# Optimization experiments

Hardware: AMD Instinct MI355X
Metric: run time of the kernel (lower is better)

Reference implementation:

```python
import jax, jax.numpy as jnp
import numpy as np

L1, L2, B, D = 512, 512, 32, 768
EPS = 1e-8

def setup_inputs() -> dict:
    key = jax.random.key(0)
    k1, k2 = jax.random.split(key)
    return {
        "x1": jax.random.normal(k1, (L1, B, D), dtype=jnp.float32),
        "x1_mask": jnp.ones((L1, B), dtype=jnp.float32),
        "x2": jax.random.normal(k2, (L2, B, D), dtype=jnp.float32),
        "x2_mask": jnp.ones((L2, B), dtype=jnp.float32),
    }

def reference(x1, x1_mask, x2, x2_mask):
    # to batch-major: [B, L, D]
    x1b = jnp.transpose(x1, (1, 0, 2))
    x2b = jnp.transpose(x2, (1, 0, 2))
    m1 = jnp.transpose(x1_mask, (1, 0))  # [B, L1]
    m2 = jnp.transpose(x2_mask, (1, 0))  # [B, L2]

    # raw scores [B, L1, L2]
    scores = jnp.einsum('bld,bmd->blm', x1b, x2b)

    # x1 attends over x2: softmax over axis 2 with x2 mask
    w2 = jnp.exp(scores - jnp.max(scores, axis=2, keepdims=True))
    w2 = w2 * m2[:, None, :]
    alpha = w2 / (jnp.sum(w2, axis=-1, keepdims=True) + EPS)  # [B, L1, L2]
    x1_dual = jnp.einsum('blm,bmd->bld', alpha, x2b)           # [B, L1, D]

    # x2 attends over x1: stabilize with max over axis 1, then transpose
    w1 = jnp.exp(scores - jnp.max(scores, axis=1, keepdims=True))
    w1 = jnp.transpose(w1, (0, 2, 1))                          # [B, L2, L1]
    w1 = w1 * m1[:, None, :]
    beta = w1 / (jnp.sum(w1, axis=-1, keepdims=True) + EPS)    # [B, L2, L1]
    x2_dual = jnp.einsum('bml,bld->bmd', beta, x1b)            # [B, L2, D]

    # back to seq-major [L, B, D]
    return (jnp.transpose(x1_dual, (1, 0, 2)), jnp.transpose(x2_dual, (1, 0, 2)))
```

## Files before the change

kernel.cpp:

```cpp
#include <hip/hip_runtime.h>

#define LQ  512
#define LKN 512
#define BB  32
#define DD  768

typedef float    f4     __attribute__((ext_vector_type(4)));
typedef _Float16 half8  __attribute__((ext_vector_type(8)));
typedef _Float16 half4  __attribute__((ext_vector_type(4)));
typedef __fp16   fp16x2 __attribute__((ext_vector_type(2)));

union H8 { half8 h; unsigned int u[4]; };

__device__ __forceinline__ unsigned int pk2(float a, float b) {
    union { fp16x2 h; unsigned int u; } c;
    c.h = __builtin_amdgcn_cvt_pkrtz(a, b);
    return c.u;
}
__device__ __forceinline__ half8 cvt8(f4 a, f4 b) {
    H8 r;
    r.u[0] = pk2(a[0], a[1]); r.u[1] = pk2(a[2], a[3]);
    r.u[2] = pk2(b[0], b[1]); r.u[3] = pk2(b[2], b[3]);
    return r.h;
}

__device__ __forceinline__ void gload16(half8& dst, const _Float16* p) {
    asm volatile("global_load_dwordx4 %0, %1, off" : "=v"(dst) : "v"(p));
}
__device__ __forceinline__ void gloadf4(f4& dst, const float* p) {
    asm volatile("global_load_dwordx4 %0, %1, off" : "=v"(dst) : "v"(p));
}

__global__ __launch_bounds__(256)
void prep_pack(const float* __restrict__ x1, const float* __restrict__ x2,
               _Float16* __restrict__ xf1, _Float16* __restrict__ xf2,
               _Float16* __restrict__ xv1, _Float16* __restrict__ xv2)
{
    const int bi   = blockIdx.x;
    const int side = bi / 1536;
    const int rem  = bi % 1536;
    const int b    = rem / 48;
    const int rem2 = rem % 48;
    const int l0   = (rem2 / 6) * 64;
    const int d0   = (rem2 % 6) * 128;

    const float* __restrict__ X  = side ? x2  : x1;
    _Float16* __restrict__    XF = side ? xf2 : xf1;
    _Float16* __restrict__    XV = side ? xv2 : xv1;

    __shared__ _Float16 T[64][136];

    const int tid = threadIdx.x;
    {
        const int r  = tid >> 4;
        const int c8 = (tid & 15) * 8;
        const float* src = X + ((size_t)(l0 + r) * BB + b) * DD + d0 + c8;
        f4 v[8];
        #pragma unroll
        for (int k = 0; k < 4; ++k) {
            gloadf4(v[2 * k],     src + (size_t)k * 16 * BB * DD);
            gloadf4(v[2 * k + 1], src + (size_t)k * 16 * BB * DD + 4);
        }
        asm volatile("s_waitcnt vmcnt(4)" ::: "memory");
        __builtin_amdgcn_sched_barrier(0);
        #pragma unroll
        for (int k = 0; k < 2; ++k) {
            half4 ha, hb;
            ha[0] = (_Float16)v[2*k][0]; ha[1] = (_Float16)v[2*k][1];
            ha[2] = (_Float16)v[2*k][2]; ha[3] = (_Float16)v[2*k][3];
            hb[0] = (_Float16)v[2*k+1][0]; hb[1] = (_Float16)v[2*k+1][1];
            hb[2] = (_Float16)v[2*k+1][2]; hb[3] = (_Float16)v[2*k+1][3];
            *(half4*)&T[r + 16 * k][c8]     = ha;
            *(half4*)&T[r + 16 * k][c8 + 4] = hb;
        }
        asm volatile("s_waitcnt vmcnt(0)" ::: "memory");
        __builtin_amdgcn_sched_barrier(0);
        #pragma unroll
        for (int k = 2; k < 4; ++k) {
            half4 ha, hb;
            ha[0] = (_Float16)v[2*k][0]; ha[1] = (_Float16)v[2*k][1];
            ha[2] = (_Float16)v[2*k][2]; ha[3] = (_Float16)v[2*k][3];
            hb[0] = (_Float16)v[2*k+1][0]; hb[1] = (_Float16)v[2*k+1][1];
            hb[2] = (_Float16)v[2*k+1][2]; hb[3] = (_Float16)v[2*k+1][3];
            *(half4*)&T[r + 16 * k][c8]     = ha;
            *(half4*)&T[r + 16 * k][c8 + 4] = hb;
        }
    }
    __syncthreads();
    #pragma unroll
    for (int c2 = tid; c2 < 1024; c2 += 256) {
        const int dhalf = c2 >> 9;
        const int t16l  = (c2 >> 7) & 3;
        const int ksl   = (c2 >> 6) & 1;
        const int ln    = c2 & 63;
        half8 v = *(const half8*)&T[t16l * 16 + (ln & 15)][dhalf * 64 + ksl * 32 + (ln >> 4) * 8];
        const size_t t16g = (size_t)(l0 >> 4) + t16l;
        const size_t ksg  = (size_t)(d0 >> 5) + dhalf * 2 + ksl;
        *(half8*)(XF + (((size_t)b * 32 + t16g) * 24 + ksg) * 512 + ln * 8) = v;
    }
    #pragma unroll
    for (int c2 = tid; c2 < 1024; c2 += 256) {
        const int dtl  = c2 >> 7;
        const int ks2l = (c2 >> 6) & 1;
        const int ln   = c2 & 63;
        half8 v;
        #pragma unroll
        for (int jj = 0; jj < 8; ++jj)
            v[jj] = T[ks2l * 32 + (ln >> 4) * 8 + jj][dtl * 16 + (ln & 15)];
        const size_t dtg  = (size_t)(d0 >> 4) + dtl;
        const size_t ks2g = (size_t)(l0 >> 5) + ks2l;
        *(half8*)(XV + (((size_t)b * 48 + dtg) * 16 + ks2g) * 512 + ln * 8) = v;
    }
}

__global__ __launch_bounds__(256, 3)
void gemm_s(const _Float16* __restrict__ xf1, const _Float16* __restrict__ xf2,
            float* __restrict__ S)
{
    const int i   = blockIdx.x;
    const int xcd = i & 7;
    const int j   = i >> 3;
    const int t   = j & 15;
    const int b   = xcd * 4 + (j >> 4);
    const int lt  = t >> 2, mt = t & 3;
    const int l0b = lt * 128, m0b = mt * 128;

    const int tid  = threadIdx.x;
    const int lane = tid & 63;
    const int w    = tid >> 6;
    const int wl   = w >> 1, wm = w & 1;
    const int lr   = lane & 15;
    const int lg   = lane >> 4;

    f4 acc[16];
    #pragma unroll
    for (int t2 = 0; t2 < 16; ++t2) acc[t2] = f4{0.f, 0.f, 0.f, 0.f};

    {
        const _Float16* ab = xf1 + (((size_t)b * 32 + lt * 8 + wl * 4) * 24) * 512 + lane * 8;
        const _Float16* bb = xf2 + (((size_t)b * 32 + mt * 8 + wm * 4) * 24) * 512 + lane * 8;
        __builtin_amdgcn_s_setprio(1);
        #pragma unroll
        for (int ks = 0; ks < 24; ++ks) {
            half8 aF[4], bF[4];
            #pragma unroll
            for (int q = 0; q < 4; ++q) {
                aF[q] = *(const half8*)(ab + ((size_t)q * 24 + ks) * 512);
                bF[q] = *(const half8*)(bb + ((size_t)q * 24 + ks) * 512);
            }
            #pragma unroll
            for (int q = 0; q < 4; ++q)
                #pragma unroll
                for (int p = 0; p < 4; ++p)
                    acc[q * 4 + p] = __builtin_amdgcn_mfma_f32_16x16x32_f16(aF[q], bF[p], acc[q * 4 + p], 0, 0, 0);
        }
        __builtin_amdgcn_s_setprio(0);
    }

    {
        float* srow = S + ((size_t)b * 512 + l0b + wl * 64) * 512 + m0b + wm * 64;
        #pragma unroll
        for (int q = 0; q < 4; ++q)
            #pragma unroll
            for (int p = 0; p < 4; ++p)
                #pragma unroll
                for (int r = 0; r < 4; ++r)
                    srow[(size_t)(q * 16 + 4 * lg + r) * 512 + p * 16 + lr] = acc[q * 4 + p][r];
    }
}

__global__ __launch_bounds__(256)
void softmax_both(const float* __restrict__ S32, float* __restrict__ PF0,
                  float* __restrict__ PF1,
                  const float* __restrict__ m1, const float* __restrict__ m2)
{
    const int bi   = blockIdx.x;
    const int side = bi >> 9;
    const int idx  = bi & 511;
    const int b    = idx >> 4;
    const int t    = idx & 15;

    const int tid  = threadIdx.x;

    if (side == 0) {
        const int lane = tid & 63;
        const int w    = tid >> 6;
        __shared__ float mask_r[LKN];
        mask_r[tid] = m2[tid * BB + b];
        mask_r[tid + 256] = m2[(tid + 256) * BB + b];
        __syncthreads();

        float mk[8];
        #pragma unroll
        for (int j = 0; j < 8; ++j) mk[j] = mask_r[lane * 8 + j];

        const int row0 = t * 32 + w * 8;

        f4 fa[8], fb[8];
        #pragma unroll
        for (int rr = 0; rr < 8; ++rr) {
            const float* rp = S32 + ((size_t)b * 512 + row0 + rr) * 512 + lane * 8;
            fa[rr] = *(const f4*)rp;
            fb[rr] = *(const f4*)(rp + 4);
        }

        #pragma unroll
        for (int rr = 0; rr < 8; ++rr) {
            float f[8] = {fa[rr][0], fa[rr][1], fa[rr][2], fa[rr][3],
                          fb[rr][0], fb[rr][1], fb[rr][2], fb[rr][3]};
            float m = fmaxf(fmaxf(fmaxf(f[0], f[1]), fmaxf(f[2], f[3])),
                            fmaxf(fmaxf(f[4], f[5]), fmaxf(f[6], f[7])));
            #pragma unroll
            for (int d = 1; d <= 32; d <<= 1) m = fmaxf(m, __shfl_xor(m, d));
            float e[8], s = 0.f;
            #pragma unroll
            for (int j = 0; j < 8; ++j) { e[j] = __expf(f[j] - m) * mk[j]; s += e[j]; }
            #pragma unroll
            for (int d = 1; d <= 32; d <<= 1) s += __shfl_xor(s, d);
            const float inv = 1.f / (s + 1e-8f);
            H8 o;
            o.u[0] = pk2(e[0] * inv, e[1] * inv); o.u[1] = pk2(e[2] * inv, e[3] * inv);
            o.u[2] = pk2(e[4] * inv, e[5] * inv); o.u[3] = pk2(e[6] * inv, e[7] * inv);
            const int row = row0 + rr;
            char* base = (char*)PF0 + ((size_t)b * 32 + (row >> 4)) * 16384;
            *(half8*)(base + (lane >> 2) * 1024 + (lane & 3) * 256 + (row & 15) * 16) = o.h;
        }
    } else {
        __shared__ float raw[32][513];
        __shared__ float mask_c[LKN];
        __shared__ float redm[8][32];
        __shared__ float reds[8][32];

        mask_c[tid] = m1[tid * BB + b];
        mask_c[tid + 256] = m1[(tid + 256) * BB + b];

        {
            const float* sbase = S32 + ((size_t)b * 512 + (tid >> 3)) * 512 + t * 32 + (tid & 7) * 4;
            f4 vv[16];
            #pragma unroll
            for (int it = 0; it < 8; ++it) gloadf4(vv[it], sbase + (size_t)it * 32 * 512);
            asm volatile("s_waitcnt vmcnt(0)" ::: "memory");
            __builtin_amdgcn_sched_barrier(0);
            #pragma unroll
            for (int it = 8; it < 16; ++it) gloadf4(vv[it], sbase + (size_t)it * 32 * 512);
            #pragma unroll
            for (int it = 0; it < 8; ++it) {
                const int row = it * 32 + (tid >> 3);
                const int c0  = (tid & 7) * 4;
                raw[c0 + 0][row] = vv[it][0]; raw[c0 + 1][row] = vv[it][1];
                raw[c0 + 2][row] = vv[it][2]; raw[c0 + 3][row] = vv[it][3];
            }
            asm volatile("s_waitcnt vmcnt(0)" ::: "memory");
            __builtin_amdgcn_sched_barrier(0);
            #pragma unroll
            for (int it = 8; it < 16; ++it) {
                const int row = it * 32 + (tid >> 3);
                const int c0  = (tid & 7) * 4;
                raw[c0 + 0][row] = vv[it][0]; raw[c0 + 1][row] = vv[it][1];
                raw[c0 + 2][row] = vv[it][2]; raw[c0 + 3][row] = vv[it][3];
            }
        }
        __syncthreads();

        const int col = tid & 31;
        const int seg = tid >> 5;

        float m = -3.0e38f;
        #pragma unroll
        for (int r = 0; r < 64; ++r) m = fmaxf(m, raw[col][seg * 64 + r]);
        redm[seg][col] = m;
        __syncthreads();
        float M = redm[0][col];
        #pragma unroll
        for (int s2 = 1; s2 < 8; ++s2) M = fmaxf(M, redm[s2][col]);

        float s = 0.f;
        #pragma unroll
        for (int r = 0; r < 64; ++r) {
            const int row = seg * 64 + r;
            s += __expf(raw[col][row] - M) * mask_c[row];
        }
        reds[seg][col] = s;
        __syncthreads();
        float L = 0.f;
        #pragma unroll
        for (int s2 = 0; s2 < 8; ++s2) L += reds[s2][col];
        const float inv = 1.f / (L + 1e-8f);

        const int col_g = t * 32 + col;
        char* pfb = (char*)PF1 + ((size_t)b * 32 + (col_g >> 4)) * 16384;
        #pragma unroll
        for (int kc = 0; kc < 8; ++kc) {
            const int k0 = seg * 64 + kc * 8;
            float e[8];
            #pragma unroll
            for (int j = 0; j < 8; ++j)
                e[j] = __expf(raw[col][k0 + j] - M) * mask_c[k0 + j] * inv;
            H8 o;
            o.u[0] = pk2(e[0], e[1]); o.u[1] = pk2(e[2], e[3]);
            o.u[2] = pk2(e[4], e[5]); o.u[3] = pk2(e[6], e[7]);
            const int lw = seg * 8 + kc;
            *(half8*)(pfb + (lw >> 2) * 1024 + (lw & 3) * 256 + (col_g & 15) * 16) = o.h;
        }
    }
}

__global__ __launch_bounds__(256)
void pv_frag(const float* __restrict__ PF0, const float* __restrict__ PF1,
             const _Float16* __restrict__ xv1, const _Float16* __restrict__ xv2,
             float* __restrict__ o1, float* __restrict__ o2)
{
    const int i    = blockIdx.x;
    const int xcd  = i & 7;
    const int j    = i >> 3;
    const int lt   = j & 3;
    const int dq   = (j >> 2) & 3;
    const int side = (j >> 4) & 1;
    const int b    = xcd * 4 + (j >> 5);
    const int l0   = lt * 128;

    const float* __restrict__ PF    = side ? PF1 : PF0;
    const _Float16* __restrict__ VF = side ? xv1 : xv2;
    float* __restrict__ OUT         = side ? o2 : o1;

    const int tid  = threadIdx.x;
    const int lane = tid & 63;
    const int w    = tid >> 6;
    const int lr   = lane & 15;
    const int lg   = lane >> 4;

    const char* pb[8];
    #pragma unroll
    for (int q = 0; q < 8; ++q)
        pb[q] = (const char*)PF + ((size_t)b * 32 + lt * 8 + q) * 16384 + lane * 16;
    const _Float16* vbase = VF + (((size_t)b * 48 + dq * 12 + w * 3) * 16) * 512 + lane * 8;

    f4 acc[24];
    #pragma unroll
    for (int t = 0; t < 24; ++t) acc[t] = f4{0.f, 0.f, 0.f, 0.f};

    half8 pa[2][8], vf[2][3];

    #pragma unroll
    for (int q = 0; q < 8; ++q) gload16(pa[0][q], (const _Float16*)(pb[q]));
    #pragma unroll
    for (int nt = 0; nt < 3; ++nt) gload16(vf[0][nt], vbase + (size_t)nt * 16 * 512);

    #pragma unroll
    for (int ks2 = 0; ks2 < 16; ++ks2) {
        const int cur = ks2 & 1;
        const int nxt = cur ^ 1;
        if (ks2 < 15) {
            #pragma unroll
            for (int q = 0; q < 8; ++q)
                gload16(pa[nxt][q], (const _Float16*)(pb[q] + (ks2 + 1) * 1024));
            #pragma unroll
            for (int nt = 0; nt < 3; ++nt)
                gload16(vf[nxt][nt], vbase + ((size_t)nt * 16 + ks2 + 1) * 512);
            asm volatile("s_waitcnt vmcnt(11)" ::: "memory");
        } else {
            asm volatile("s_waitcnt vmcnt(0)" ::: "memory");
        }
        __builtin_amdgcn_sched_barrier(0);
        __builtin_amdgcn_s_setprio(1);
        #pragma unroll
        for (int nt = 0; nt < 3; ++nt)
            #pragma unroll
            for (int q = 0; q < 8; ++q)
                acc[q * 3 + nt] = __builtin_amdgcn_mfma_f32_16x16x32_f16(pa[cur][q], vf[cur][nt], acc[q * 3 + nt], 0, 0, 0);
        __builtin_amdgcn_s_setprio(0);
    }

    #pragma unroll
    for (int q = 0; q < 8; ++q)
        #pragma unroll
        for (int nt = 0; nt < 3; ++nt)
            #pragma unroll
            for (int r = 0; r < 4; ++r)
                OUT[((size_t)(l0 + q * 16 + 4 * lg + r) * BB + b) * DD + dq * 192 + (w * 3 + nt) * 16 + lr]
                    = acc[q * 3 + nt][r];
}

__global__ __launch_bounds__(256)
void coatt_flash_f32(const float* __restrict__ x1, const float* __restrict__ m1,
                     const float* __restrict__ x2, const float* __restrict__ m2,
                     float* __restrict__ o1, float* __restrict__ o2)
{
    const int i    = blockIdx.x;
    const int xcd  = i & 7;
    const int j    = i >> 3;
    const int pair = xcd * 8 + (j >> 5);
    const int qt   = j & 31;
    const int side = pair >> 5;
    const int b    = pair & 31;

    const float* __restrict__ Q   = side ? x2 : x1;
    const float* __restrict__ K   = side ? x1 : x2;
    const float* __restrict__ MK  = side ? m1 : m2;
    float* __restrict__       OUT = side ? o2 : o1;

    const int tid  = threadIdx.x;
    const int lane = tid & 63;
    const int w    = tid >> 6;
    const int lr   = lane & 15;
    const int lg   = lane >> 4;
    const int q0 = qt * 16;
    const int d0 = w * (DD / 4);

    __shared__ float sred[4][16][36];
    __shared__ float mask_s[LKN];
    for (int t = tid; t < LKN; t += 256) mask_s[t] = MK[t * BB + b];

    half8 qf[6];
    {
        const float* qrow = Q + ((q0 + lr) * BB + b) * DD + d0 + lg * 8;
        #pragma unroll
        for (int ks = 0; ks < 6; ++ks) {
            f4 a = *(const f4*)(qrow + ks * 32);
            f4 c = *(const f4*)(qrow + ks * 32 + 4);
            qf[ks] = cvt8(a, c);
        }
    }
    f4 acc[12];
    #pragma unroll
    for (int t = 0; t < 12; ++t) acc[t] = f4{0.f, 0.f, 0.f, 0.f};
    float Mrun = -3.0e38f, Lrun = 0.f;
    for (int kt = 0; kt < 16; ++kt) {
        const int k0 = kt * 32;
        f4 s0 = {0.f,0.f,0.f,0.f}, s1 = {0.f,0.f,0.f,0.f};
        {
            const float* kb0 = K + ((k0 + lr) * BB + b) * DD + d0 + lg * 8;
            const float* kb1 = kb0 + 16 * BB * DD;
            #pragma unroll
            for (int ks = 0; ks < 6; ++ks) {
                f4 a0 = *(const f4*)(kb0 + ks * 32);
                f4 c0 = *(const f4*)(kb0 + ks * 32 + 4);
                s0 = __builtin_amdgcn_mfma_f32_16x16x32_f16(qf[ks], cvt8(a0, c0), s0, 0, 0, 0);
                f4 a1 = *(const f4*)(kb1 + ks * 32);
                f4 c1 = *(const f4*)(kb1 + ks * 32 + 4);
                s1 = __builtin_amdgcn_mfma_f32_16x16x32_f16(qf[ks], cvt8(a1, c1), s1, 0, 0, 0);
            }
        }
        __syncthreads();
        #pragma unroll
        for (int r = 0; r < 4; ++r) {
            sred[w][4 * lg + r][lr]      = s0[r];
            sred[w][4 * lg + r][16 + lr] = s1[r];
        }
        __syncthreads();
        f4 sa = {0.f,0.f,0.f,0.f}, sb = {0.f,0.f,0.f,0.f};
        #pragma unroll
        for (int ww = 0; ww < 4; ++ww) {
            sa += *(const f4*)&sred[ww][lr][lg * 8];
            sb += *(const f4*)&sred[ww][lr][lg * 8 + 4];
        }
        float tmax = fmaxf(fmaxf(fmaxf(sa[0], sa[1]), fmaxf(sa[2], sa[3])),
                           fmaxf(fmaxf(sb[0], sb[1]), fmaxf(sb[2], sb[3])));
        tmax = fmaxf(tmax, __shfl_xor(tmax, 16));
        tmax = fmaxf(tmax, __shfl_xor(tmax, 32));
        const float Mnew  = fmaxf(Mrun, tmax);
        const float scale = __expf(Mrun - Mnew);
        float p[8];
        float psum = 0.f;
        const float* mrow = &mask_s[k0 + lg * 8];
        #pragma unroll
        for (int t = 0; t < 4; ++t) { p[t]     = __expf(sa[t] - Mnew) * mrow[t];     psum += p[t]; }
        #pragma unroll
        for (int t = 0; t < 4; ++t) { p[4 + t] = __expf(sb[t] - Mnew) * mrow[4 + t]; psum += p[4 + t]; }
        psum += __shfl_xor(psum, 16);
        psum += __shfl_xor(psum, 32);
        Lrun = Lrun * scale + psum;
        Mrun = Mnew;
        H8 pf;
        pf.u[0] = pk2(p[0], p[1]); pf.u[1] = pk2(p[2], p[3]);
        pf.u[2] = pk2(p[4], p[5]); pf.u[3] = pk2(p[6], p[7]);
        float sc[4];
        #pragma unroll
        for (int r = 0; r < 4; ++r) sc[r] = __shfl(scale, (lane & 48) + 4 * lg + r);
        #pragma unroll
        for (int t = 0; t < 12; ++t) {
            acc[t][0] *= sc[0]; acc[t][1] *= sc[1];
            acc[t][2] *= sc[2]; acc[t][3] *= sc[3];
        }
        const float* vb = K + ((k0 + lg * 8) * BB + b) * DD + d0 + lr;
        #pragma unroll
        for (int nt = 0; nt < 12; ++nt) {
            const float* vp = vb + nt * 16;
            float vv[8];
            #pragma unroll
            for (int t = 0; t < 8; ++t) vv[t] = vp[t * BB * DD];
            H8 vf;
            vf.u[0] = pk2(vv[0], vv[1]); vf.u[1] = pk2(vv[2], vv[3]);
            vf.u[2] = pk2(vv[4], vv[5]); vf.u[3] = pk2(vv[6], vv[7]);
            acc[nt] = __builtin_amdgcn_mfma_f32_16x16x32_f16(pf.h, vf.h, acc[nt], 0, 0, 0);
        }
    }
    float il[4];
    {
        const float inv = 1.f / (Lrun + 1e-8f);
        #pragma unroll
        for (int r = 0; r < 4; ++r) il[r] = __shfl(inv, (lane & 48) + 4 * lg + r);
    }
    #pragma unroll
    for (int nt = 0; nt < 12; ++nt) {
        #pragma unroll
        for (int r = 0; r < 4; ++r) {
            OUT[((q0 + 4 * lg + r) * BB + b) * DD + d0 + nt * 16 + lr] = acc[nt][r] * il[r];
        }
    }
}

extern "C" void kernel_launch(void* const* d_in, const int* in_sizes, int n_in,
                              void* d_out, int out_size, void* d_ws, size_t ws_size,
                              hipStream_t stream) {
    (void)in_sizes; (void)n_in; (void)out_size;
    const float* x1 = (const float*)d_in[0];
    const float* m1 = (const float*)d_in[1];
    const float* x2 = (const float*)d_in[2];
    const float* m2 = (const float*)d_in[3];
    float* o1 = (float*)d_out;
    float* o2 = o1 + (size_t)LQ * BB * DD;

    const size_t ELEMS = (size_t)LQ * BB * DD;
    const size_t SELEM = (size_t)BB * 512 * 512;
    const size_t NEED  = 4 * ELEMS * sizeof(_Float16)
                       + SELEM * sizeof(float);

    if (ws_size >= NEED) {
        _Float16* xf1 = (_Float16*)d_ws;
        _Float16* xf2 = xf1 + ELEMS;
        _Float16* xv1 = xf2 + ELEMS;
        _Float16* xv2 = xv1 + ELEMS;
        float*    S32 = (float*)(xv2 + ELEMS);
        float*    PF0 = (float*)d_ws;
        float*    PF1 = (float*)((char*)d_ws + (size_t)32 * 32 * 16384);
        prep_pack<<<3072, 256, 0, stream>>>(x1, x2, xf1, xf2, xv1, xv2);
        gemm_s<<<512, 256, 0, stream>>>(xf1, xf2, S32);
        softmax_both<<<1024, 256, 0, stream>>>(S32, PF0, PF1, m1, m2);
        pv_frag<<<1024, 256, 0, stream>>>(PF0, PF1, xv1, xv2, o1, o2);
    } else {
        coatt_flash_f32<<<2048, 256, 0, stream>>>(x1, m1, x2, m2, o1, o2);
    }
}
```

Measured before the change: 133.2 us.

## Share P tiles across waves through double-buffered LDS instead of redundant global loads

In the P·V output kernel, all four waves used to load the same eight P fragments from global memory. Now each wave loads only two fragments per k-step, writes them to a double-buffered shared-memory tile, and every wave reads all eight back from LDS. The aim is to cut redundant global and L2 traffic for P by a factor of four. The cost is an LDS round trip and a block-wide barrier on every iteration, which may reduce overlap between loads and MFMA work.

```diff
diff --git a/kernel.cpp b/kernel.cpp
--- a/kernel.cpp
+++ b/kernel.cpp
@@ -329,46 +329,66 @@
     const int lr   = lane & 15;
     const int lg   = lane >> 4;
 
-    const char* pb[8];
-    #pragma unroll
-    for (int q = 0; q < 8; ++q)
-        pb[q] = (const char*)PF + ((size_t)b * 32 + lt * 8 + q) * 16384 + lane * 16;
+    __shared__ char plds[2][8192];
+
+    const char* psA = (const char*)PF + ((size_t)b * 32 + lt * 8 + 2 * w)     * 16384 + lane * 16;
+    const char* psB = (const char*)PF + ((size_t)b * 32 + lt * 8 + 2 * w + 1) * 16384 + lane * 16;
     const _Float16* vbase = VF + (((size_t)b * 48 + dq * 12 + w * 3) * 16) * 512 + lane * 8;
 
     f4 acc[24];
     #pragma unroll
     for (int t = 0; t < 24; ++t) acc[t] = f4{0.f, 0.f, 0.f, 0.f};
 
-    half8 pa[2][8], vf[2][3];
-
-    #pragma unroll
-    for (int q = 0; q < 8; ++q) gload16(pa[0][q], (const _Float16*)(pb[q]));
+    half8 vf[2][3];
+    half8 pA, pB;
+
+    gload16(pA, (const _Float16*)psA);
+    gload16(pB, (const _Float16*)psB);
+    asm volatile("s_waitcnt vmcnt(0)" ::: "memory");
+    __builtin_amdgcn_sched_barrier(0);
+    *(half8*)(plds[0] + (2 * w) * 1024 + lane * 16)     = pA;
+    *(half8*)(plds[0] + (2 * w + 1) * 1024 + lane * 16) = pB;
     #pragma unroll
     for (int nt = 0; nt < 3; ++nt) gload16(vf[0][nt], vbase + (size_t)nt * 16 * 512);
+    __syncthreads();
 
     #pragma unroll
     for (int ks2 = 0; ks2 < 16; ++ks2) {
         const int cur = ks2 & 1;
         const int nxt = cur ^ 1;
+
+        half8 pa[8];
+        #pragma unroll
+        for (int q = 0; q < 8; ++q)
+            pa[q] = *(const half8*)(plds[cur] + q * 1024 + lane * 16);
+
         if (ks2 < 15) {
-            #pragma unroll
-            for (int q = 0; q < 8; ++q)
-                gload16(pa[nxt][q], (const _Float16*)(pb[q] + (ks2 + 1) * 1024));
+            gload16(pA, (const _Float16*)(psA + (ks2 + 1) * 1024));
+            gload16(pB, (const _Float16*)(psB + (ks2 + 1) * 1024));
             #pragma unroll
             for (int nt = 0; nt < 3; ++nt)
                 gload16(vf[nxt][nt], vbase + ((size_t)nt * 16 + ks2 + 1) * 512);
-            asm volatile("s_waitcnt vmcnt(11)" ::: "memory");
+            asm volatile("s_waitcnt vmcnt(5)" ::: "memory");
         } else {
             asm volatile("s_waitcnt vmcnt(0)" ::: "memory");
         }
         __builtin_amdgcn_sched_barrier(0);
+
         __builtin_amdgcn_s_setprio(1);
         #pragma unroll
         for (int nt = 0; nt < 3; ++nt)
             #pragma unroll
             for (int q = 0; q < 8; ++q)
-                acc[q * 3 + nt] = __builtin_amdgcn_mfma_f32_16x16x32_f16(pa[cur][q], vf[cur][nt], acc[q * 3 + nt], 0, 0, 0);
+                acc[q * 3 + nt] = __builtin_amdgcn_mfma_f32_16x16x32_f16(pa[q], vf[cur][nt], acc[q * 3 + nt], 0, 0, 0);
         __builtin_amdgcn_s_setprio(0);
+
+        if (ks2 < 15) {
+            asm volatile("s_waitcnt vmcnt(3)" ::: "memory");
+            __builtin_amdgcn_sched_barrier(0);
+            *(half8*)(plds[nxt] + (2 * w) * 1024 + lane * 16)     = pA;
+            *(half8*)(plds[nxt] + (2 * w + 1) * 1024 + lane * 16) = pB;
+        }
+        __syncthreads();
     }
 
     #pragma unroll
```

Result: no change. 131.1 us (-1.6%).
